# Kernel optimization log

Hardware: AMD Instinct MI355X
Metric: run time of the kernel (lower is better)

The kernel has to match this reference:

```python
import jax, jax.numpy as jnp
import numpy as np

OUT = 2048        # weight_size[0]
IN_BASE = 2048    # original input features
N_EMBED = 64      # replacements per iteration
IN_TOT = IN_BASE + 2 * N_EMBED  # 2176, weight_size[1]
NNZ_W = 400000
NNZ_B = 1024
BATCH = 8192


def setup_inputs() -> dict:
    key = jax.random.key(0)
    ks = jax.random.split(key, 10)
    return {
        "x": jax.random.normal(ks[0], (BATCH, IN_BASE), dtype=jnp.float32),
        "weight_vals": jax.random.normal(ks[1], (NNZ_W,), dtype=jnp.float32),
        "weight_rows": jax.random.randint(ks[2], (NNZ_W,), 0, OUT, dtype=jnp.int32),
        "weight_cols": jax.random.randint(ks[3], (NNZ_W,), 0, IN_TOT, dtype=jnp.int32),
        "bias_vals": jax.random.normal(ks[4], (NNZ_B,), dtype=jnp.float32),
        "bias_idx": jax.random.randint(ks[5], (NNZ_B,), 0, OUT, dtype=jnp.int32),
        "embed0_vals": jax.random.uniform(ks[6], (N_EMBED,), dtype=jnp.float32),
        "embed0_parents": jax.random.randint(ks[7], (N_EMBED,), 0, IN_BASE, dtype=jnp.int32),
        "embed1_vals": jax.random.uniform(ks[8], (N_EMBED,), dtype=jnp.float32),
        "embed1_parents": jax.random.randint(ks[9], (N_EMBED,), 0, IN_BASE + N_EMBED, dtype=jnp.int32),
    }


def reference(x, weight_vals, weight_rows, weight_cols, bias_vals, bias_idx,
              embed0_vals, embed0_parents, embed1_vals, embed1_parents):
    # EmbedLinear layers: each appends one new feature per stored row,
    # new_feat[:, c] = value[c] * x[:, parent[c]]  (single nnz per sparse row)
    x = jnp.concatenate([x, x[:, embed0_parents] * embed0_vals[None, :]], axis=1)  # [B, 2112]
    x = jnp.concatenate([x, x[:, embed1_parents] * embed1_vals[None, :]], axis=1)  # [B, 2176]
    # sparse weight -> dense via scatter-add (coalesce semantics sum duplicates)
    W = jnp.zeros((OUT, IN_TOT), dtype=weight_vals.dtype).at[weight_rows, weight_cols].add(weight_vals)
    b = jnp.zeros((OUT,), dtype=bias_vals.dtype).at[bias_idx].add(bias_vals)
    # (W @ x^T)^T + b  ==  x @ W^T + b
    return x @ W.T + b[None, :]
```

## Files before the change

kernel.cpp:

```cpp
#include <hip/hip_runtime.h>
#include <stdint.h>

#define OUT_F   2048
#define IN_BASE 2048
#define N_EMB   64
#define IN_TOT  2176
#define NNZ_W   400000
#define NNZ_B   1024
#define BATCH   8192

typedef __bf16 bf16x8 __attribute__((ext_vector_type(8)));
typedef __bf16 bf16x4 __attribute__((ext_vector_type(4)));
typedef float  floatx16 __attribute__((ext_vector_type(16)));

#define AS1 __attribute__((address_space(1)))
#define AS3 __attribute__((address_space(3)))

#define NB_BUILD (BATCH * (IN_TOT / 4) / 256)
#define NB_SCAT  ((NNZ_W + NNZ_B + 255) / 256)

__global__ void __launch_bounds__(256) prep_kernel(
    const float* __restrict__ x,
    const float* __restrict__ e0v, const int* __restrict__ e0p,
    const float* __restrict__ e1v, const int* __restrict__ e1p,
    __bf16* __restrict__ xb,
    const float* __restrict__ wv, const int* __restrict__ wr,
    const int* __restrict__ wc,
    const float* __restrict__ bv, const int* __restrict__ bi,
    float* __restrict__ Wf, float* __restrict__ bfp)
{
    if (blockIdx.x < NB_BUILD) {
        const int GROUPS = IN_TOT / 4;
        int gid = blockIdx.x * 256 + threadIdx.x;
        int b = gid / GROUPS;
        int g = gid - b * GROUPS;
        const float* xr = x + (size_t)b * IN_BASE;

        float v[4];
        if (g < IN_BASE / 4) {
            const float4 t = *(const float4*)(xr + g * 4);
            v[0] = t.x; v[1] = t.y; v[2] = t.z; v[3] = t.w;
        } else if (g < (IN_BASE + N_EMB) / 4) {
            int j = (g - IN_BASE / 4) * 4;
#pragma unroll
            for (int t = 0; t < 4; t++) v[t] = e0v[j + t] * xr[e0p[j + t]];
        } else {
            int j = (g - (IN_BASE + N_EMB) / 4) * 4;
#pragma unroll
            for (int t = 0; t < 4; t++) {
                int p = e1p[j + t];
                float base = (p < IN_BASE) ? xr[p]
                                           : e0v[p - IN_BASE] * xr[e0p[p - IN_BASE]];
                v[t] = e1v[j + t] * base;
            }
        }
        bf16x4 o;
        o[0] = (__bf16)v[0]; o[1] = (__bf16)v[1]; o[2] = (__bf16)v[2]; o[3] = (__bf16)v[3];
        *(bf16x4*)(xb + (size_t)b * IN_TOT + g * 4) = o;
    } else {
        int i = (blockIdx.x - NB_BUILD) * 256 + threadIdx.x;
        if (i < NNZ_W) {
            unsafeAtomicAdd(Wf + (size_t)wr[i] * IN_TOT + wc[i], wv[i]);
        } else if (i < NNZ_W + NNZ_B) {
            int j = i - NNZ_W;
            unsafeAtomicAdd(bfp + bi[j], bv[j]);
        }
    }
}

__global__ void __launch_bounds__(256) w_to_bf16_kernel(
    const float* __restrict__ Wf, __bf16* __restrict__ Wb)
{
    int e = (blockIdx.x * 256 + threadIdx.x) * 4;
    const float4 t = *(const float4*)(Wf + e);
    bf16x4 o;
    o[0] = (__bf16)t.x; o[1] = (__bf16)t.y; o[2] = (__bf16)t.z; o[3] = (__bf16)t.w;
    *(bf16x4*)(Wb + e) = o;
}

#define BM 256
#define BN 256
#define BK 64
#define NKT (IN_TOT / BK)
static_assert(NKT % 2 == 0, "pipeline consumes K-tiles in pairs");

#define CFENCE asm volatile("" ::: "memory")
#define BAR do { CFENCE; __builtin_amdgcn_s_barrier(); CFENCE; } while (0)
#define VMW(n) asm volatile("s_waitcnt vmcnt(" #n ")" ::: "memory")
#define NOPS do {} while (0)

#define STAGE(G, SBC, buf, tile, half) do {                                     \
    const __bf16* _s = (G) + (size_t)((half) * 128) * IN_TOT + (tile) * 64;     \
    char* _d = (SBC) + (buf) * 32768 + (half) * 16384 + tid * 16;               \
    __builtin_amdgcn_global_load_lds((AS1 void*)(uintptr_t)_s,                  \
                                     (AS3 void*)_d, 16, 0, 0);                  \
    __builtin_amdgcn_global_load_lds((AS1 void*)(uintptr_t)(_s + (size_t)64 * IN_TOT), \
                                     (AS3 void*)(_d + 8192), 16, 0, 0);         \
} while (0)

#define RD_A(pA, mq) do {                                                       \
    _Pragma("unroll") for (int ks = 0; ks < 4; ks++) {                          \
        const int kc = ks * 2 + khalf;                                          \
        _Pragma("unroll") for (int mi = 0; mi < 2; mi++) {                      \
            const int r = (mq) * 128 + wm * 64 + mi * 32 + l32;                 \
            a[mi * 4 + ks] = *(const bf16x8*)((pA) + r * 64 + ((kc ^ (r & 7)) * 8)); \
        }                                                                       \
    }                                                                           \
} while (0)

#define RD_B(pB, nq, barr) do {                                                 \
    _Pragma("unroll") for (int ks = 0; ks < 4; ks++) {                          \
        const int kc = ks * 2 + khalf;                                          \
        const int rb = (nq) * 128 + wn * 32 + l32;                              \
        barr[ks] = *(const bf16x8*)((pB) + rb * 64 + ((kc ^ (rb & 7)) * 8));    \
    }                                                                           \
} while (0)

#define MMPH(mq, nq, barr) do {                                                 \
    BAR;                                                                        \
    __builtin_amdgcn_s_setprio(1);                                              \
    _Pragma("unroll") for (int mi = 0; mi < 2; mi++)                            \
        _Pragma("unroll") for (int ks = 0; ks < 4; ks++)                        \
            acc[mq][mi][nq] = __builtin_amdgcn_mfma_f32_32x32x16_bf16(          \
                a[mi * 4 + ks], barr[ks], acc[mq][mi][nq], 0, 0, 0);            \
    __builtin_amdgcn_s_setprio(0);                                              \
    BAR;                                                                        \
} while (0)

#define KTILE(buf, STG1, STG2, STG3, STG4, W4) do {                             \
    const __bf16* _pA = sA + (buf) * 16384;                                     \
    const __bf16* _pB = sB + (buf) * 16384;                                     \
    RD_A(_pA, 0); RD_B(_pB, 0, b0);                                             \
    STG1;              MMPH(0, 0, b0);                                          \
    RD_B(_pB, 1, b1);                                                           \
    STG2;              MMPH(0, 1, b1);                                          \
    RD_A(_pA, 1);                                                               \
    STG3;              MMPH(1, 1, b1);                                          \
    STG4; W4;          MMPH(1, 0, b0);                                          \
} while (0)

__global__ void __launch_bounds__(512, 2) gemm_kernel(
    const __bf16* __restrict__ A,
    const __bf16* __restrict__ W,
    const float*  __restrict__ bias,
    float* __restrict__ C)
{
    __shared__ __align__(16) __bf16 sA[2 * 256 * 64];
    __shared__ __align__(16) __bf16 sB[2 * 256 * 64];

    const int tid   = threadIdx.x;
    const int bm    = blockIdx.x;
    const int bn    = blockIdx.y;
    const int wave  = tid >> 6;
    const int lane  = tid & 63;
    const int wm    = wave >> 2;
    const int wn    = wave & 3;
    const int l32   = lane & 31;
    const int khalf = lane >> 5;

    floatx16 acc[2][2][2] = {};
    bf16x8 a[8];
    bf16x8 b0[4], b1[4];

    const int srow   = tid >> 3;
    const int kchunk = ((tid & 7) ^ ((tid >> 3) & 7)) * 8;
    const __bf16* Ag = A + (size_t)(bm * BM + srow) * IN_TOT + kchunk;
    const __bf16* Wg = W + (size_t)(bn * BN + srow) * IN_TOT + kchunk;
    char* sAc = (char*)sA;
    char* sBc = (char*)sB;

    STAGE(Ag, sAc, 0, 0, 0);
    STAGE(Ag, sAc, 0, 0, 1);
    STAGE(Wg, sBc, 0, 0, 0);
    STAGE(Wg, sBc, 0, 0, 1);
    STAGE(Ag, sAc, 1, 1, 0);
    STAGE(Wg, sBc, 1, 1, 1);
    VMW(4);
    BAR;

#pragma unroll 1
    for (int i = 0; i < NKT / 2 - 1; ++i) {
        const int t1 = 2 * i + 1, t2 = 2 * i + 2, t3 = 2 * i + 3;
        KTILE(0, STAGE(Ag, sAc, 1, t1, 1), STAGE(Wg, sBc, 1, t1, 0),
                 STAGE(Ag, sAc, 0, t2, 0), STAGE(Wg, sBc, 0, t2, 1), VMW(4));
        KTILE(1, STAGE(Ag, sAc, 0, t2, 1), STAGE(Wg, sBc, 0, t2, 0),
                 STAGE(Ag, sAc, 1, t3, 0), STAGE(Wg, sBc, 1, t3, 1), VMW(4));
    }
    KTILE(0, STAGE(Ag, sAc, 1, NKT - 1, 1), STAGE(Wg, sBc, 1, NKT - 1, 0),
             NOPS, NOPS, VMW(0));
    KTILE(1, NOPS, NOPS, NOPS, NOPS, NOPS);

#pragma unroll
    for (int m = 0; m < 2; m++)
#pragma unroll
    for (int mi = 0; mi < 2; mi++)
#pragma unroll
    for (int n = 0; n < 2; n++) {
        const int colg = bn * BN + n * 128 + wn * 32 + l32;
        const float bvv = bias[colg];
        const int rowb = bm * BM + m * 128 + wm * 64 + mi * 32 + 4 * khalf;
#pragma unroll
        for (int reg = 0; reg < 16; reg++) {
            const int rowg = rowb + (reg & 3) + 8 * (reg >> 2);
            C[(size_t)rowg * OUT_F + colg] = acc[m][mi][n][reg] + bvv;
        }
    }
}

extern "C" void kernel_launch(void* const* d_in, const int* in_sizes, int n_in,
                              void* d_out, int out_size, void* d_ws, size_t ws_size,
                              hipStream_t stream) {
    const float* x      = (const float*)d_in[0];
    const float* w_vals = (const float*)d_in[1];
    const int*   w_rows = (const int*)  d_in[2];
    const int*   w_cols = (const int*)  d_in[3];
    const float* b_vals = (const float*)d_in[4];
    const int*   b_idx  = (const int*)  d_in[5];
    const float* e0v    = (const float*)d_in[6];
    const int*   e0p    = (const int*)  d_in[7];
    const float* e1v    = (const float*)d_in[8];
    const int*   e1p    = (const int*)  d_in[9];
    float* out = (float*)d_out;

    char* ws = (char*)d_ws;
    const size_t W_F32_BYTES  = (size_t)OUT_F * IN_TOT * 4;
    const size_t B_F32_BYTES  = (size_t)OUT_F * 4;
    const size_t W_BF16_BYTES = (size_t)OUT_F * IN_TOT * 2;
    float*  Wf = (float*)ws;
    float*  bfp = (float*)(ws + W_F32_BYTES);
    __bf16* Wb = (__bf16*)(ws + W_F32_BYTES + B_F32_BYTES);
    __bf16* xb = (__bf16*)(ws + W_F32_BYTES + B_F32_BYTES + W_BF16_BYTES);

    hipMemsetAsync(Wf, 0, W_F32_BYTES + B_F32_BYTES, stream);

    prep_kernel<<<NB_BUILD + NB_SCAT, 256, 0, stream>>>(
        x, e0v, e0p, e1v, e1p, xb,
        w_vals, w_rows, w_cols, b_vals, b_idx, Wf, bfp);

    w_to_bf16_kernel<<<((size_t)OUT_F * IN_TOT / 4) / 256, 256, 0, stream>>>(Wf, Wb);

    dim3 grid(BATCH / BM, OUT_F / BN);
    gemm_kernel<<<grid, 512, 0, stream>>>(xb, Wb, bfp, out);
}
```

Baseline: 231.8 us.

## Scatter weights directly into bf16 with packed atomics and drop conversion pass

Sparse weight entries are now accumulated straight into the bf16 weight matrix with global_atomic_pk_add_bf16, which removes the fp32 weight buffer, its larger memset, and the separate fp32-to-bf16 conversion kernel. The x-build part of the prep kernel also changes to one block per batch row with simple vectorised passes and only 32 threads doing the embedding gathers, which avoids per-thread divisions and branch divergence. The cost is that duplicate weight entries are summed in bf16 instead of fp32, so accuracy drops where several entries share a position.

```diff
diff --git a/kernel.cpp b/kernel.cpp
--- a/kernel.cpp
+++ b/kernel.cpp
@@ -16,7 +16,7 @@
 #define AS1 __attribute__((address_space(1)))
 #define AS3 __attribute__((address_space(3)))
 
-#define NB_BUILD (BATCH * (IN_TOT / 4) / 256)
+#define NB_BUILD BATCH
 #define NB_SCAT  ((NNZ_W + NNZ_B + 255) / 256)
 
 __global__ void __launch_bounds__(256) prep_kernel(
@@ -27,55 +27,64 @@
     const float* __restrict__ wv, const int* __restrict__ wr,
     const int* __restrict__ wc,
     const float* __restrict__ bv, const int* __restrict__ bi,
-    float* __restrict__ Wf, float* __restrict__ bfp)
+    __bf16* __restrict__ Wb, float* __restrict__ bfp)
 {
+    const int tid = threadIdx.x;
     if (blockIdx.x < NB_BUILD) {
-        const int GROUPS = IN_TOT / 4;
-        int gid = blockIdx.x * 256 + threadIdx.x;
-        int b = gid / GROUPS;
-        int g = gid - b * GROUPS;
+        const int b = blockIdx.x;
         const float* xr = x + (size_t)b * IN_BASE;
-
-        float v[4];
-        if (g < IN_BASE / 4) {
+        __bf16* xo = xb + (size_t)b * IN_TOT;
+
+#pragma unroll
+        for (int pass = 0; pass < 2; pass++) {
+            const int g = pass * 256 + tid;
             const float4 t = *(const float4*)(xr + g * 4);
-            v[0] = t.x; v[1] = t.y; v[2] = t.z; v[3] = t.w;
-        } else if (g < (IN_BASE + N_EMB) / 4) {
-            int j = (g - IN_BASE / 4) * 4;
-#pragma unroll
-            for (int t = 0; t < 4; t++) v[t] = e0v[j + t] * xr[e0p[j + t]];
-        } else {
-            int j = (g - (IN_BASE + N_EMB) / 4) * 4;
-#pragma unroll
-            for (int t = 0; t < 4; t++) {
-                int p = e1p[j + t];
-                float base = (p < IN_BASE) ? xr[p]
-                                           : e0v[p - IN_BASE] * xr[e0p[p - IN_BASE]];
-                v[t] = e1v[j + t] * base;
+            bf16x4 o;
+            o[0] = (__bf16)t.x; o[1] = (__bf16)t.y;
+            o[2] = (__bf16)t.z; o[3] = (__bf16)t.w;
+            *(bf16x4*)(xo + g * 4) = o;
+        }
+        if (tid < 32) {
+            const int g = 512 + tid;
+            float v[4];
+            if (g < 528) {
+                const int j = (g - 512) * 4;
+#pragma unroll
+                for (int t = 0; t < 4; t++) v[t] = e0v[j + t] * xr[e0p[j + t]];
+            } else {
+                const int j = (g - 528) * 4;
+#pragma unroll
+                for (int t = 0; t < 4; t++) {
+                    const int p = e1p[j + t];
+                    const float base = (p < IN_BASE)
+                        ? xr[p]
+                        : e0v[p - IN_BASE] * xr[e0p[p - IN_BASE]];
+                    v[t] = e1v[j + t] * base;
+                }
             }
-        }
-        bf16x4 o;
-        o[0] = (__bf16)v[0]; o[1] = (__bf16)v[1]; o[2] = (__bf16)v[2]; o[3] = (__bf16)v[3];
-        *(bf16x4*)(xb + (size_t)b * IN_TOT + g * 4) = o;
+            bf16x4 o;
+            o[0] = (__bf16)v[0]; o[1] = (__bf16)v[1];
+            o[2] = (__bf16)v[2]; o[3] = (__bf16)v[3];
+            *(bf16x4*)(xo + g * 4) = o;
+        }
     } else {
-        int i = (blockIdx.x - NB_BUILD) * 256 + threadIdx.x;
+        const int i = (blockIdx.x - NB_BUILD) * 256 + tid;
         if (i < NNZ_W) {
-            unsafeAtomicAdd(Wf + (size_t)wr[i] * IN_TOT + wc[i], wv[i]);
+            const int r = wr[i], c = wc[i];
+            const size_t idx = (size_t)r * IN_TOT + c;
+            const __bf16 h = (__bf16)wv[i];
+            const unsigned short hb = __builtin_bit_cast(unsigned short, h);
+            const unsigned int data = (idx & 1) ? ((unsigned int)hb << 16)
+                                                : (unsigned int)hb;
+            const uint64_t addr = (uint64_t)(uintptr_t)(Wb + (idx & ~(size_t)1));
+            asm volatile("global_atomic_pk_add_bf16 %0, %1, off"
+                         :: "v"(addr), "v"(data) : "memory");
         } else if (i < NNZ_W + NNZ_B) {
-            int j = i - NNZ_W;
+            const int j = i - NNZ_W;
             unsafeAtomicAdd(bfp + bi[j], bv[j]);
         }
+        asm volatile("s_waitcnt vmcnt(0)" ::: "memory");
     }
-}
-
-__global__ void __launch_bounds__(256) w_to_bf16_kernel(
-    const float* __restrict__ Wf, __bf16* __restrict__ Wb)
-{
-    int e = (blockIdx.x * 256 + threadIdx.x) * 4;
-    const float4 t = *(const float4*)(Wf + e);
-    bf16x4 o;
-    o[0] = (__bf16)t.x; o[1] = (__bf16)t.y; o[2] = (__bf16)t.z; o[3] = (__bf16)t.w;
-    *(bf16x4*)(Wb + e) = o;
 }
 
 #define BM 256
@@ -223,21 +232,17 @@
     float* out = (float*)d_out;
 
     char* ws = (char*)d_ws;
-    const size_t W_F32_BYTES  = (size_t)OUT_F * IN_TOT * 4;
+    const size_t W_BF16_BYTES = (size_t)OUT_F * IN_TOT * 2;
     const size_t B_F32_BYTES  = (size_t)OUT_F * 4;
-    const size_t W_BF16_BYTES = (size_t)OUT_F * IN_TOT * 2;
-    float*  Wf = (float*)ws;
-    float*  bfp = (float*)(ws + W_F32_BYTES);
-    __bf16* Wb = (__bf16*)(ws + W_F32_BYTES + B_F32_BYTES);
-    __bf16* xb = (__bf16*)(ws + W_F32_BYTES + B_F32_BYTES + W_BF16_BYTES);
-
-    hipMemsetAsync(Wf, 0, W_F32_BYTES + B_F32_BYTES, stream);
+    __bf16* Wb  = (__bf16*)ws;
+    float*  bfp = (float*)(ws + W_BF16_BYTES);
+    __bf16* xb  = (__bf16*)(ws + W_BF16_BYTES + B_F32_BYTES);
+
+    hipMemsetAsync(Wb, 0, W_BF16_BYTES + B_F32_BYTES, stream);
 
     prep_kernel<<<NB_BUILD + NB_SCAT, 256, 0, stream>>>(
         x, e0v, e0p, e1v, e1p, xb,
-        w_vals, w_rows, w_cols, b_vals, b_idx, Wf, bfp);
-
-    w_to_bf16_kernel<<<((size_t)OUT_F * IN_TOT / 4) / 256, 256, 0, stream>>>(Wf, Wb);
+        w_vals, w_rows, w_cols, b_vals, b_idx, Wb, bfp);
 
     dim3 grid(BATCH / BM, OUT_F / BN);
     gemm_kernel<<<grid, 512, 0, stream>>>(xb, Wb, bfp, out);
```

Measured after the change: 220.1 us. 5.0% less time.
